# Kernel optimization log

Hardware: AMD Instinct MI355X
Metric: run time of the kernel (lower is better)

Reference implementation:

```python
import jax, jax.numpy as jnp
import numpy as np

M = 65536
INPUT_DIM = 16
OUTPUT_DIM = 64
N = 32          # coordinates transformed by the spline
K = 16          # number of spline bins
MIN_BW = 0.001  # DEFAULT_MIN_BIN_WIDTH
MIN_BH = 0.001  # DEFAULT_MIN_BIN_HEIGHT


def setup_inputs() -> dict:
    key = jax.random.key(0)
    k1, k2, k3, k4 = jax.random.split(key, 4)
    c = jax.random.uniform(k1, (M, INPUT_DIM), jnp.float32)
    z = jax.random.uniform(k2, (M, OUTPUT_DIM), jnp.float32)  # data in [0,1] spline domain
    s_in = OUTPUT_DIM - N + INPUT_DIM  # 48
    s_out = N * (2 * K + 1)            # 1056
    W = jax.random.normal(k3, (s_in, s_out), jnp.float32) * 0.05
    b = jax.random.normal(k4, (s_out,), jnp.float32) * 0.05
    return {"c": c, "z": z, "W": W, "b": b}


def _quadratic_spline(inputs, unnormalized_widths, unnormalized_heights):
    # inputs: [m, n] in [0,1]; unnormalized_widths: [m, n, K]; unnormalized_heights: [m, n, K+1]
    num_bins = unnormalized_widths.shape[-1]

    widths = jax.nn.softmax(unnormalized_widths, axis=-1)
    widths = MIN_BW + (1.0 - MIN_BW * num_bins) * widths

    h = jax.nn.softplus(unnormalized_heights) + 0.001  # [m, n, K+1]
    # (heights have K+1 = num_bins+1 knots, so the 'num_bins-1' padding branch is skipped)
    area = jnp.sum((h[..., :-1] + h[..., 1:]) * 0.5 * widths, axis=-1, keepdims=True)
    heights = h / area
    heights = MIN_BH + (1.0 - MIN_BH) * heights

    cdf = jnp.cumsum((heights[..., :-1] + heights[..., 1:]) * 0.5 * widths, axis=-1)
    cdf = cdf.at[..., -1].set(1.0)
    bin_left_cdf = jnp.pad(cdf, ((0, 0), (0, 0), (1, 0)))  # [m, n, K+1]

    locs = jnp.cumsum(widths, axis=-1).at[..., -1].set(1.0)
    bin_locations = jnp.pad(locs, ((0, 0), (0, 0), (1, 0)))  # [m, n, K+1]

    # nflows torchutils.searchsorted: bump last knot by eps, count knots <= input
    locs_eps = bin_locations.at[..., -1].add(1e-6)
    bin_idx = jnp.sum(inputs[..., None] >= locs_eps, axis=-1) - 1  # [m, n] int

    def gather(arr, idx):
        return jnp.take_along_axis(arr, idx[..., None], axis=-1)[..., 0]

    input_bin_locations = gather(bin_locations, bin_idx)
    input_bin_widths = gather(widths, bin_idx)
    input_left_cdf = gather(bin_left_cdf, bin_idx)
    input_left_heights = gather(heights, bin_idx)
    input_right_heights = gather(heights, bin_idx + 1)

    a = 0.5 * (input_right_heights - input_left_heights) * input_bin_widths
    bq = input_left_heights * input_bin_widths
    cq = input_left_cdf

    alpha = (inputs - input_bin_locations) / input_bin_widths
    outputs = jnp.clip(a * alpha ** 2 + bq * alpha + cq, 0.0, 1.0)
    logabsdet = jnp.log(alpha * (input_right_heights - input_left_heights) + input_left_heights)
    return outputs, logabsdet


def reference(c, z, W, b):
    # forward (reverse=False) branch of QuadraticsSpline.forward
    z1, z2 = z[:, :N], z[:, N:]
    z2c = jnp.concatenate([z2, c], axis=1)
    y = z2c @ W + b                                  # conditioner s (linear)
    sv = y.reshape(y.shape[0], N, 2 * K + 1)
    unnormalized_heights = sv[..., : K + 1]          # first split chunk (size K+1)
    unnormalized_widths = sv[..., K + 1:]            # second chunk (size K)
    x1, log_det = _quadratic_spline(z1, unnormalized_widths, unnormalized_heights)
    x = jnp.concatenate([z2, x1], axis=1)            # note: original concatenates (x2, x1)
    return x, log_det.sum(axis=1)
```

## Files before the change

### kernel.cpp

```cpp
#include <hip/hip_runtime.h>
#include <hip/hip_bf16.h>
#include <math.h>

#define M_ROWS 65536
#define NSPLINE 32
#define BM 64
#define WROWS 16
#define GROUP 4
#define NITER (NSPLINE / GROUP)
#define YS 40
#define WB_ELEMS (32 * 3 * 2 * 64 * 8)

typedef __attribute__((ext_vector_type(8))) _Float16 half8;
typedef __attribute__((ext_vector_type(4))) _Float16 half4;
typedef __attribute__((ext_vector_type(4))) float floatx4;

__device__ __forceinline__ float softplus_fast(float t) {
    float u = t * t;
    if (u > 1.21f) return log1pf(__expf(t));
    float p = fmaf(u, -2.6352e-5f, 3.4722222e-4f);
    p = fmaf(u, p, -5.2083333e-3f);
    p = fmaf(u, p, 0.125f);
    p = fmaf(u, p, 0.69314718f);
    return fmaf(t, 0.5f, p);
}

__global__ void pack_W(const float* __restrict__ W, const float* __restrict__ b,
                       _Float16* __restrict__ WH) {
    int idx = blockIdx.x * 256 + threadIdx.x;
    int j    = idx & 7;
    int lane = (idx >> 3) & 63;
    int half = (idx >> 9) & 1;
    int tmp  = idx >> 10;
    int t    = tmp % 3;
    int sp   = tmp / 3;
    int k  = half * 32 + ((lane >> 4) << 3) + j;
    int cl = t * 16 + (lane & 15);
    float v = 0.0f;
    if (cl < 33 && k <= 48) {
        int col = sp * 33 + cl;
        v = (k < 48) ? W[k * 1056 + col] : b[col];
    }
    WH[idx] = (_Float16)v;
}

__global__ void __launch_bounds__(256) fused_kernel(
    const float* __restrict__ z, const float* __restrict__ c,
    const _Float16* __restrict__ WH, float* __restrict__ out)
{
    __shared__ _Float16 lds_y[4 * 64 * YS];

    const int tid  = threadIdx.x;
    const int w    = tid >> 6;
    const int lane = tid & 63;
    const int q    = lane >> 4;
    const int cc   = lane & 15;
    const int row_base = blockIdx.x * BM + w * WROWS;
    _Float16* lds_wv = lds_y + w * (64 * YS);

    #pragma unroll
    for (int it = 0; it < 2; ++it) {
        int idx = it * 64 + lane;
        int rr  = row_base + (idx >> 3);
        int v4  = idx & 7;
        float4 val = *(const float4*)(z + (size_t)rr * 64 + 32 + v4 * 4);
        *(float4*)(out + (size_t)rr * 64 + v4 * 4) = val;
    }

    half8 a0, a1;
    {
        const float* zr = z + (size_t)(row_base + cc) * 64 + 32;
        float4 v0 = *(const float4*)(zr + q * 8);
        float4 v1 = *(const float4*)(zr + q * 8 + 4);
        a0[0]=(_Float16)v0.x; a0[1]=(_Float16)v0.y;
        a0[2]=(_Float16)v0.z; a0[3]=(_Float16)v0.w;
        a0[4]=(_Float16)v1.x; a0[5]=(_Float16)v1.y;
        a0[6]=(_Float16)v1.z; a0[7]=(_Float16)v1.w;
        if (q < 2) {
            const float* cr = c + (size_t)(row_base + cc) * 16 + q * 8;
            float4 u0 = *(const float4*)cr;
            float4 u1 = *(const float4*)(cr + 4);
            a1[0]=(_Float16)u0.x; a1[1]=(_Float16)u0.y;
            a1[2]=(_Float16)u0.z; a1[3]=(_Float16)u0.w;
            a1[4]=(_Float16)u1.x; a1[5]=(_Float16)u1.y;
            a1[6]=(_Float16)u1.z; a1[7]=(_Float16)u1.w;
        } else {
            #pragma unroll
            for (int j = 0; j < 8; ++j) a1[j] = (_Float16)0.0f;
            if (q == 2) a1[0] = (_Float16)1.0f;
        }
    }

    float ld_acc = 0.0f;

    #pragma unroll 1
    for (int g = 0; g < NITER; ++g) {
        __syncthreads();

        #pragma unroll
        for (int sp = 0; sp < GROUP; ++sp) {
            const int spg = g * GROUP + sp;
            const int task = sp * 16 + cc;
            #pragma unroll
            for (int t = 0; t < 3; ++t) {
                const half8* p = (const half8*)WH + (size_t)(spg * 3 + t) * 128 + lane;
                half8 b0 = p[0];
                half8 b1 = p[64];
                floatx4 acc = {0.f, 0.f, 0.f, 0.f};
                acc = __builtin_amdgcn_mfma_f32_16x16x32_f16(b0, a0, acc, 0, 0, 0);
                acc = __builtin_amdgcn_mfma_f32_16x16x32_f16(b1, a1, acc, 0, 0, 0);
                if (t < 2) {
                    half4 v;
                    v[0] = (_Float16)acc[0]; v[1] = (_Float16)acc[1];
                    v[2] = (_Float16)acc[2]; v[3] = (_Float16)acc[3];
                    *(half4*)(lds_wv + task * YS + t * 16 + q * 4) = v;
                } else if (q == 0) {
                    lds_wv[task * YS + 32] = (_Float16)acc[0];
                }
            }
        }
        __syncthreads();

        const int n = g * GROUP + q;
        const _Float16* my = lds_wv + (q * 16 + cc) * YS;
        const half8* mp = (const half8*)my;
        half8 r0 = mp[0], r1 = mp[1], r2 = mp[2], r3 = mp[3];
        float pv[33];
        #pragma unroll
        for (int i = 0; i < 8; ++i) pv[i]      = (float)r0[i];
        #pragma unroll
        for (int i = 0; i < 8; ++i) pv[8 + i]  = (float)r1[i];
        #pragma unroll
        for (int i = 0; i < 8; ++i) pv[16 + i] = (float)r2[i];
        #pragma unroll
        for (int i = 0; i < 8; ++i) pv[24 + i] = (float)r3[i];
        pv[32] = (float)my[32];

        const float in = z[(size_t)(row_base + cc) * 64 + n];

        float wd[16];
        float sew = 0.f;
        #pragma unroll
        for (int i = 0; i < 16; ++i) {
            float e = __expf(pv[17 + i]);
            wd[i] = e; sew += e;
        }
        const float inv_sew = 0.984f / sew;
        #pragma unroll
        for (int i = 0; i < 16; ++i) wd[i] = 0.001f + wd[i] * inv_sew;

        float h[17];
        #pragma unroll
        for (int i = 0; i < 17; ++i)
            h[i] = softplus_fast(pv[i]) + 0.001f;

        float area = 0.f;
        #pragma unroll
        for (int i = 0; i < 16; ++i) area += (h[i] + h[i + 1]) * 0.5f * wd[i];
        const float inv_area = 0.999f / area;
        #pragma unroll
        for (int i = 0; i < 17; ++i) h[i] = 0.001f + h[i] * inv_area;

        float loc = 0.f, cdfl = 0.f;
        float sel_loc = 0.f, sel_w = wd[0], sel_cdf = 0.f;
        float sel_lh = h[0], sel_rh = h[1];
        #pragma unroll
        for (int bn = 1; bn < 16; ++bn) {
            cdfl = fmaf((h[bn - 1] + h[bn]) * 0.5f, wd[bn - 1], cdfl);
            loc += wd[bn - 1];
            if (in >= loc) {
                sel_loc = loc; sel_w = wd[bn]; sel_cdf = cdfl;
                sel_lh = h[bn]; sel_rh = h[bn + 1];
            }
        }

        const float alpha = (in - sel_loc) / sel_w;
        const float dh    = sel_rh - sel_lh;
        float o = ((0.5f * dh * sel_w) * alpha + sel_lh * sel_w) * alpha + sel_cdf;
        o = fminf(fmaxf(o, 0.0f), 1.0f);
        out[(size_t)(row_base + cc) * 64 + 32 + n] = o;
        ld_acc += __logf(fmaf(alpha, dh, sel_lh));
    }

    ld_acc += __shfl_down(ld_acc, 32, 64);
    ld_acc += __shfl_down(ld_acc, 16, 64);
    if (q == 0)
        out[(size_t)M_ROWS * 64 + row_base + cc] = ld_acc;
}

extern "C" void kernel_launch(void* const* d_in, const int* in_sizes, int n_in,
                              void* d_out, int out_size, void* d_ws, size_t ws_size,
                              hipStream_t stream) {
    const float* c = (const float*)d_in[0];
    const float* z = (const float*)d_in[1];
    const float* W = (const float*)d_in[2];
    const float* b = (const float*)d_in[3];
    float* out = (float*)d_out;
    _Float16* WH = (_Float16*)d_ws;

    pack_W<<<WB_ELEMS / 256, 256, 0, stream>>>(W, b, WH);
    fused_kernel<<<M_ROWS / BM, 256, 0, stream>>>(z, c, WH, out);
}
```

Before: 122.4 us.

## Drop block barriers, stage fp32 conditioner outputs in LDS, preload spline inputs

Each wave writes and reads only its own LDS region, so the two block-wide __syncthreads per iteration are removed and the wave relies on intra-wave ordering instead. The MFMA results are now stored to LDS as fp32 with a 34-float row stride, which avoids the fp16 conversions and changes the bank mapping. The eight z inputs each lane needs are loaded into registers before the loop rather than loaded from global memory on every iteration. In exchange, LDS use per block grows by about 70 percent, and register pressure rises from the preloaded inputs, which could lower occupancy.

```diff
diff --git a/kernel.cpp b/kernel.cpp
--- a/kernel.cpp
+++ b/kernel.cpp
@@ -8,11 +8,10 @@
 #define WROWS 16
 #define GROUP 4
 #define NITER (NSPLINE / GROUP)
-#define YS 40
+#define YS 34
 #define WB_ELEMS (32 * 3 * 2 * 64 * 8)
 
 typedef __attribute__((ext_vector_type(8))) _Float16 half8;
-typedef __attribute__((ext_vector_type(4))) _Float16 half4;
 typedef __attribute__((ext_vector_type(4))) float floatx4;
 
 __device__ __forceinline__ float softplus_fast(float t) {
@@ -48,7 +47,7 @@
     const float* __restrict__ z, const float* __restrict__ c,
     const _Float16* __restrict__ WH, float* __restrict__ out)
 {
-    __shared__ _Float16 lds_y[4 * 64 * YS];
+    __shared__ float lds_y[4 * 64 * YS];
 
     const int tid  = threadIdx.x;
     const int w    = tid >> 6;
@@ -56,7 +55,7 @@
     const int q    = lane >> 4;
     const int cc   = lane & 15;
     const int row_base = blockIdx.x * BM + w * WROWS;
-    _Float16* lds_wv = lds_y + w * (64 * YS);
+    float* lds_wv = lds_y + w * (64 * YS);
 
     #pragma unroll
     for (int it = 0; it < 2; ++it) {
@@ -91,12 +90,17 @@
         }
     }
 
+    float zin[NITER];
+    {
+        const float* zr = z + (size_t)(row_base + cc) * 64 + q;
+        #pragma unroll
+        for (int g = 0; g < NITER; ++g) zin[g] = zr[g * 4];
+    }
+
     float ld_acc = 0.0f;
 
     #pragma unroll 1
     for (int g = 0; g < NITER; ++g) {
-        __syncthreads();
-
         #pragma unroll
         for (int sp = 0; sp < GROUP; ++sp) {
             const int spg = g * GROUP + sp;
@@ -110,33 +114,26 @@
                 acc = __builtin_amdgcn_mfma_f32_16x16x32_f16(b0, a0, acc, 0, 0, 0);
                 acc = __builtin_amdgcn_mfma_f32_16x16x32_f16(b1, a1, acc, 0, 0, 0);
                 if (t < 2) {
-                    half4 v;
-                    v[0] = (_Float16)acc[0]; v[1] = (_Float16)acc[1];
-                    v[2] = (_Float16)acc[2]; v[3] = (_Float16)acc[3];
-                    *(half4*)(lds_wv + task * YS + t * 16 + q * 4) = v;
+                    float* dst = lds_wv + task * YS + t * 16 + q * 4;
+                    *(float2*)dst       = make_float2(acc[0], acc[1]);
+                    *(float2*)(dst + 2) = make_float2(acc[2], acc[3]);
                 } else if (q == 0) {
-                    lds_wv[task * YS + 32] = (_Float16)acc[0];
+                    lds_wv[task * YS + 32] = acc[0];
                 }
             }
         }
-        __syncthreads();
 
         const int n = g * GROUP + q;
-        const _Float16* my = lds_wv + (q * 16 + cc) * YS;
-        const half8* mp = (const half8*)my;
-        half8 r0 = mp[0], r1 = mp[1], r2 = mp[2], r3 = mp[3];
+        const float* my = lds_wv + lane * YS;
         float pv[33];
         #pragma unroll
-        for (int i = 0; i < 8; ++i) pv[i]      = (float)r0[i];
-        #pragma unroll
-        for (int i = 0; i < 8; ++i) pv[8 + i]  = (float)r1[i];
-        #pragma unroll
-        for (int i = 0; i < 8; ++i) pv[16 + i] = (float)r2[i];
-        #pragma unroll
-        for (int i = 0; i < 8; ++i) pv[24 + i] = (float)r3[i];
-        pv[32] = (float)my[32];
-
-        const float in = z[(size_t)(row_base + cc) * 64 + n];
+        for (int i = 0; i < 16; ++i) {
+            float2 v = *(const float2*)(my + 2 * i);
+            pv[2 * i] = v.x; pv[2 * i + 1] = v.y;
+        }
+        pv[32] = my[32];
+
+        const float in = zin[g];
 
         float wd[16];
         float sew = 0.f;
```

After: 118.7 us. 1.03x faster.
